# Performance work log

Hardware: AMD Instinct MI355X
Metric: run time of the kernel (lower is better)

The kernel has to match this reference:

```python
import jax, jax.numpy as jnp
import numpy as np

D_MODEL = 512
N_HEADS = 8
HEAD_DIM = D_MODEL // N_HEADS          # 64
ROTARY_DIM = HEAD_DIM // 2             # 32 (rotary_frac = 0.5)
MAX_SEQ_LEN = 512
EPS = 1e-6


def _rope_tables(seq_len, dtype=jnp.float32):
    inv_freq = 1.0 / (10000.0 ** (jnp.arange(0, ROTARY_DIM, 2, dtype=jnp.float32) / ROTARY_DIM))
    t = jnp.arange(seq_len, dtype=jnp.float32)
    freqs = jnp.outer(t, inv_freq)          # (T, ROTARY_DIM//2)
    return jnp.sin(freqs).astype(dtype), jnp.cos(freqs).astype(dtype)


def _apply_rope(x, sin, cos):
    # x: (R, H, T, Dh); rotate interleaved pairs of the first ROTARY_DIM dims
    rd = ROTARY_DIM
    x1 = x[..., :rd].reshape(*x.shape[:-1], rd // 2, 2)
    x2 = x[..., rd:]
    s = sin[None, None, :, :]
    c = cos[None, None, :, :]
    a, b = x1[..., 0], x1[..., 1]
    rot = jnp.stack([a * c - b * s, a * s + b * c], axis=-1).reshape(*x.shape[:-1], rd)
    return jnp.concatenate([rot, x2], axis=-1)


def setup_inputs() -> dict:
    key = jax.random.key(0)
    ks = jax.random.split(key, 8)
    B, T, N, D = 1, 384, 128, D_MODEL
    x = jax.random.normal(ks[0], (B, T, N, D), dtype=jnp.float32)
    neuron_pad_mask = jax.random.randint(ks[1], (B, N), 0, 2, dtype=jnp.int32)
    scale = 1.0 / np.sqrt(D)
    norm_w = jnp.ones((D,), dtype=jnp.float32)
    wq = jax.random.normal(ks[2], (D, D), dtype=jnp.float32) * scale
    wk = jax.random.normal(ks[3], (D, D), dtype=jnp.float32) * scale
    wv = jax.random.normal(ks[4], (D, D), dtype=jnp.float32) * scale
    wo = jax.random.normal(ks[5], (D, D), dtype=jnp.float32) * scale
    return {"x": x, "neuron_pad_mask": neuron_pad_mask, "norm_w": norm_w,
            "wq": wq, "wk": wk, "wv": wv, "wo": wo}


def reference(x, neuron_pad_mask, norm_w, wq, wk, wv, wo):
    B, T, N, D = x.shape
    H, Dh = N_HEADS, HEAD_DIM

    # RMSNorm over d_model
    xn = x * jax.lax.rsqrt(jnp.mean(x * x, axis=-1, keepdims=True) + EPS) * norm_w

    # (B,T,N,D) -> (B*N, T, D): each neuron is an independent causal timeline
    xt = jnp.transpose(xn, (0, 2, 1, 3)).reshape(B * N, T, D)
    res = xt

    # QKV projections (Linear, no bias: x @ W^T), split into heads -> (R,H,T,Dh)
    def to_bhld(y):
        return jnp.transpose(y.reshape(B * N, T, H, Dh), (0, 2, 1, 3))

    q = to_bhld(xt @ wq.T)
    k = to_bhld(xt @ wk.T)
    v = to_bhld(xt @ wv.T)

    sin, cos = _rope_tables(T, dtype=x.dtype)
    q = _apply_rope(q, sin, cos)
    k = _apply_rope(k, sin, cos)

    # Causal SDPA per row (scale = 1/sqrt(Dh), matching F.scaled_dot_product_attention)
    scores = jnp.einsum('rhtd,rhsd->rhts', q, k) / np.sqrt(Dh).astype(x.dtype)
    causal = jnp.tril(jnp.ones((T, T), dtype=bool))
    scores = jnp.where(causal[None, None], scores, jnp.finfo(scores.dtype).min)
    attn = jax.nn.softmax(scores, axis=-1)
    out = jnp.einsum('rhts,rhsd->rhtd', attn, v)            # (R,H,T,Dh)
    out = jnp.transpose(out, (0, 2, 1, 3)).reshape(B * N, T, D)

    # Only valid (non-padded) neuron rows receive attention output (others stay 0)
    valid = (neuron_pad_mask.reshape(-1) != 0)
    out = jnp.where(valid[:, None, None], out, jnp.zeros((), dtype=out.dtype))

    out = out + res
    out = jnp.transpose(out.reshape(B, N, T, D), (0, 2, 1, 3))  # (B,T,N,D)
    return out @ wo.T
```

## Files before the change

kernel.cpp:

```cpp
#include <hip/hip_runtime.h>
#include <hip/hip_bf16.h>
#include <stdint.h>

typedef __bf16 bf16x8 __attribute__((ext_vector_type(8)));
typedef float f32x4 __attribute__((ext_vector_type(4)));

static constexpr int T_SEQ  = 384;
static constexpr int NNEUR  = 128;
static constexpr int DMODEL = 512;
static constexpr int NROWS  = NNEUR * T_SEQ;
static constexpr float ROPE_C = 0.8304820237218406f;

__device__ __forceinline__ float bf2f(unsigned short u) {
  union { unsigned int i; float f; } x; x.i = ((unsigned int)u) << 16; return x.f;
}
__device__ __forceinline__ unsigned short f2bf(float f) {
  union { float f; unsigned int i; } x; x.f = f;
  unsigned int i = x.i;
  i += 0x7FFFu + ((i >> 16) & 1u);
  return (unsigned short)(i >> 16);
}
__device__ __forceinline__ float fast_exp2(float x) {
#if __has_builtin(__builtin_amdgcn_exp2f)
  return __builtin_amdgcn_exp2f(x);
#else
  return exp2f(x);
#endif
}

__device__ __forceinline__ void async_copy16(const unsigned short* g, unsigned short* l) {
  auto gp = reinterpret_cast<const __attribute__((address_space(1))) unsigned int*>(
      reinterpret_cast<uintptr_t>(g));
  auto lp = reinterpret_cast<__attribute__((address_space(3))) unsigned int*>(
      reinterpret_cast<uintptr_t>(l));
  __builtin_amdgcn_global_load_lds(gp, lp, 16, 0, 0);
}

__global__ __launch_bounds__(256) void cvt_w_kernel(
    const float* __restrict__ w0, const float* __restrict__ w1,
    const float* __restrict__ w2, const float* __restrict__ w3,
    unsigned short* __restrict__ o0, unsigned short* __restrict__ o1,
    unsigned short* __restrict__ o2, unsigned short* __restrict__ o3)
{
  const float* w; unsigned short* o;
  switch (blockIdx.y) {
    case 0:  w = w0; o = o0; break;
    case 1:  w = w1; o = o1; break;
    case 2:  w = w2; o = o2; break;
    default: w = w3; o = o3; break;
  }
  int i = (blockIdx.x * 256 + threadIdx.x) * 4;
  float4 v = *reinterpret_cast<const float4*>(w + i);
  union { unsigned short u[4]; uint2 v2; } p;
  p.u[0] = f2bf(v.x); p.u[1] = f2bf(v.y); p.u[2] = f2bf(v.z); p.u[3] = f2bf(v.w);
  *reinterpret_cast<uint2*>(o + i) = p.v2;
}

__global__ __launch_bounds__(256) void rope_tab_kernel(float2* __restrict__ tab) {
  int idx = blockIdx.x * 256 + threadIdx.x;
  int t = idx >> 4, i = idx & 15;
  float ang = (float)t * exp2f(-(float)i * ROPE_C);
  float s, c; sincosf(ang, &s, &c);
  tab[idx] = make_float2(s, c);
}

__global__ __launch_bounds__(256) void rmsnorm_kernel(
    const float* __restrict__ x, const float* __restrict__ nw,
    unsigned short* __restrict__ xt)
{
  int wave = threadIdx.x >> 6, lane = threadIdx.x & 63;
  int rid = blockIdx.x * 4 + wave;
  int t = rid >> 7, n = rid & 127;
  const float* row = x + (size_t)rid * DMODEL;
  float4 v0 = *reinterpret_cast<const float4*>(row + lane * 8);
  float4 v1 = *reinterpret_cast<const float4*>(row + lane * 8 + 4);
  float ss = v0.x*v0.x + v0.y*v0.y + v0.z*v0.z + v0.w*v0.w
           + v1.x*v1.x + v1.y*v1.y + v1.z*v1.z + v1.w*v1.w;
  #pragma unroll
  for (int off = 32; off; off >>= 1) ss += __shfl_xor(ss, off);
  float sc = rsqrtf(ss * (1.0f / DMODEL) + 1e-6f);
  float4 w0 = *reinterpret_cast<const float4*>(nw + lane * 8);
  float4 w1 = *reinterpret_cast<const float4*>(nw + lane * 8 + 4);
  union { unsigned short u[8]; uint4 v; } p;
  p.u[0] = f2bf(v0.x * sc * w0.x); p.u[1] = f2bf(v0.y * sc * w0.y);
  p.u[2] = f2bf(v0.z * sc * w0.z); p.u[3] = f2bf(v0.w * sc * w0.w);
  p.u[4] = f2bf(v1.x * sc * w1.x); p.u[5] = f2bf(v1.y * sc * w1.y);
  p.u[6] = f2bf(v1.z * sc * w1.z); p.u[7] = f2bf(v1.w * sc * w1.w);
  *reinterpret_cast<uint4*>(xt + ((size_t)n * T_SEQ + t) * DMODEL + lane * 8) = p.v;
}

template <int MODE, typename OutT>
__global__ __launch_bounds__(512, 4) void gemm_k(
    const unsigned short* __restrict__ A,
    const unsigned short* __restrict__ B,
    OutT* __restrict__ C,
    const float2* __restrict__ tab,
    const int* __restrict__ pad)
{
  __shared__ alignas(16) unsigned short Sh[2][12288];
  const int tid  = threadIdx.x;
  const int wave = tid >> 6, lane = tid & 63;
  const int l15  = lane & 15, quad = lane >> 4;
  const int wm = (wave >> 1) * 64, wn = (wave & 1) * 64;

  constexpr int GX = (MODE == 2) ? 8 : (MODE == 3) ? 2 : 4;
  constexpr int GY = (MODE == 3) ? 384 : 192;
  constexpr int NB = GX * GY;
  constexpr int CH = NB / 8;
  const int lin = (int)blockIdx.y * GX + (int)blockIdx.x;
  const int swz = (lin & 7) * CH + (lin >> 3);
  const int bx  = swz % GX, by = swz / GX;

  size_t m0; int n0;
  if constexpr (MODE == 3) { m0 = (size_t)bx * 256; n0 = by * 128; }
  else                     { m0 = (size_t)by * 256; n0 = bx * 128; }

  if constexpr (MODE == 2) {
    int nfirst = (int)(m0 / 384);
    int nlast  = (int)((m0 + 255) / 384);
    if (pad[nfirst] == 0 && pad[nlast] == 0) return;
  }
  if constexpr (MODE == 3) {
    if (pad[n0 / 384] == 0) return;
  }

  const int r4 = tid >> 2;
  const int c4 = tid & 3;
  const int gc = c4 ^ (r4 & 3);
  const unsigned short* ga = A + (m0 + r4) * 512 + gc * 8;
  const unsigned short* gb = B + ((size_t)n0 + r4) * 512 + gc * 8;

  const int pc = (quad ^ (l15 & 3)) * 8;

  auto STAGE = [&](int kk, int b) {
    const unsigned short* gak = ga + kk * 32;
    unsigned short* base = &Sh[b][0];
    async_copy16(gak,             base + tid * 8);
    async_copy16(gak + 128 * 512, base + 4096 + tid * 8);
    async_copy16(gb + kk * 32,    base + 8192 + tid * 8);
  };

  f32x4 acc[4][4] = {};
  auto COMPUTE = [&](int b) {
    const unsigned short* base = &Sh[b][0];
    bf16x8 a[4], bb[4];
    #pragma unroll
    for (int i = 0; i < 4; ++i)
      a[i] = *reinterpret_cast<const bf16x8*>(&base[(wm + i * 16 + l15) * 32 + pc]);
    #pragma unroll
    for (int j = 0; j < 4; ++j)
      bb[j] = *reinterpret_cast<const bf16x8*>(&base[8192 + (wn + j * 16 + l15) * 32 + pc]);
    #pragma unroll
    for (int i = 0; i < 4; ++i)
      #pragma unroll
      for (int j = 0; j < 4; ++j)
        acc[i][j] = __builtin_amdgcn_mfma_f32_16x16x32_bf16(a[i], bb[j], acc[i][j], 0, 0, 0);
  };

  STAGE(0, 0);
  #pragma unroll 2
  for (int kk = 0; kk < 15; ++kk) {
    const int b = kk & 1;
    STAGE(kk + 1, b ^ 1);
    asm volatile("s_waitcnt vmcnt(3)" ::: "memory");
    __builtin_amdgcn_s_barrier();
    __builtin_amdgcn_sched_barrier(0);
    COMPUTE(b);
    __builtin_amdgcn_sched_barrier(0);
    __builtin_amdgcn_s_barrier();
    __builtin_amdgcn_sched_barrier(0);
  }
  asm volatile("s_waitcnt vmcnt(0)" ::: "memory");
  __builtin_amdgcn_s_barrier();
  __builtin_amdgcn_sched_barrier(0);
  COMPUTE(1);

  if constexpr (MODE == 3) {
    #pragma unroll
    for (int j = 0; j < 4; ++j) {
      int xbase = n0 + wn + j * 16;
      int nn    = xbase / 384;
      int bloc  = xbase - nn * 384;
      int off64 = (bloc >> 6) * 64 + ((bloc >> 4) & 3);
      #pragma unroll
      for (int i = 0; i < 4; ++i)
        #pragma unroll
        for (int r = 0; r < 4; ++r) {
          int dout = (int)m0 + wm + i * 16 + quad * 4 + r;
          C[((size_t)nn * 512 + dout) * 384 + off64 + l15 * 4] = f2bf(acc[i][j][r]);
        }
    }
  } else {
    OutT* Cb = C;
    int ncol0 = n0 + wn;
    if constexpr (MODE == 2) {
      int sec = n0 >> 9;
      Cb = C + (size_t)sec * NROWS * 512;
      ncol0 = (n0 & 511) + wn;
    }
    #pragma unroll
    for (int i = 0; i < 4; ++i) {
      #pragma unroll
      for (int r = 0; r < 4; ++r) {
        size_t grow = m0 + wm + i * 16 + quad * 4 + r;
        int t = (int)(grow % 384);
        #pragma unroll
        for (int j = 0; j < 4; ++j) {
          float v = acc[i][j][r];
          int col = ncol0 + j * 16 + l15;
          if constexpr (MODE == 2) {
            if (((ncol0 + j * 16) & 63) < 32) {
              float part = __shfl_xor(v, 1);
              float2 scv = tab[t * 16 + ((col & 63) >> 1)];
              v = (l15 & 1) ? (part * scv.x + v * scv.y)
                            : (v * scv.y - part * scv.x);
            }
            Cb[grow * 512 + col] = f2bf(v);
          } else {
            Cb[grow * 512 + col] = v;
          }
        }
      }
    }
  }
}

__global__ __launch_bounds__(256, 4) void attn_kernel(
    const unsigned short* __restrict__ qb,
    const unsigned short* __restrict__ kb,
    const unsigned short* __restrict__ vt,
    const unsigned short* __restrict__ xt,
    const int* __restrict__ pad,
    unsigned short* __restrict__ y)
{
  const int lin = (int)blockIdx.x + 6 * ((int)blockIdx.y + 8 * (int)blockIdx.z);
  const int swz = (lin & 7) * 768 + (lin >> 3);
  const int qt  = swz % 6;
  const int rem = swz / 6;
  const int h   = rem & 7;
  const int n   = rem >> 3;

  const int tid  = threadIdx.x;

  if (pad[n] == 0) {
    int tq = qt * 64 + (tid >> 2);
    int d  = h * 64 + (tid & 3) * 16;
    const uint4* src = reinterpret_cast<const uint4*>(
        &xt[((size_t)n * T_SEQ + tq) * 512 + d]);
    uint4* dst = reinterpret_cast<uint4*>(
        &y[((size_t)tq * NNEUR + n) * 512 + d]);
    dst[0] = src[0];
    dst[1] = src[1];
    return;
  }

  __shared__ alignas(16) unsigned short Qs[64 * 64];
  __shared__ alignas(16) unsigned short Ks[64 * 64];
  __shared__ alignas(16) unsigned short VTs[64 * 64];
  __shared__ alignas(16) unsigned short Ps[4][16][72];

  const int wave = tid >> 6, lane = tid & 63;
  const int l15  = lane & 15, quad = lane >> 4;
  const int lrow = lane >> 3, lchunk = (lane & 7) ^ ((lane >> 3) & 7);
  const float C2 = 0.18033688011112042f;

  const unsigned short* gq =
      qb + ((size_t)n * T_SEQ + qt * 64 + wave * 16 + lrow) * 512 + h * 64 + lchunk * 8;
  async_copy16(gq,           &Qs[(wave * 16) * 64]);
  async_copy16(gq + 8 * 512, &Qs[(wave * 16 + 8) * 64]);

  const unsigned short* gk0 =
      kb + ((size_t)n * T_SEQ + wave * 16 + lrow) * 512 + h * 64 + lchunk * 8;
  const unsigned short* gv0 =
      vt + ((size_t)n * 512 + h * 64 + wave * 16 + lrow) * 384 + lchunk * 8;

  float lsum[4] = {0.f, 0.f, 0.f, 0.f};
  f32x4 oacc[4] = {};

  for (int kt = 0; kt <= qt; ++kt) {
    async_copy16(gk0 + (size_t)(kt * 64) * 512,     &Ks[(wave * 16) * 64]);
    async_copy16(gk0 + (size_t)(kt * 64 + 8) * 512, &Ks[(wave * 16 + 8) * 64]);
    async_copy16(gv0 + kt * 64,                     &VTs[(wave * 16) * 64]);
    async_copy16(gv0 + kt * 64 + 8 * 384,           &VTs[(wave * 16 + 8) * 64]);
    __syncthreads();

    f32x4 sc4[4] = {};
    #pragma unroll
    for (int kc = 0; kc < 2; ++kc) {
      const int pc = ((kc * 4 + quad) ^ (l15 & 7)) * 8;
      bf16x8 aq = *reinterpret_cast<const bf16x8*>(&Qs[(wave * 16 + l15) * 64 + pc]);
      #pragma unroll
      for (int tc = 0; tc < 4; ++tc) {
        bf16x8 bk = *reinterpret_cast<const bf16x8*>(&Ks[(tc * 16 + l15) * 64 + pc]);
        sc4[tc] = __builtin_amdgcn_mfma_f32_16x16x32_bf16(aq, bk, sc4[tc], 0, 0, 0);
      }
    }
    const bool diag = (kt == qt);
    float ps[4][4];
    #pragma unroll
    for (int tc = 0; tc < 4; ++tc)
      #pragma unroll
      for (int r = 0; r < 4; ++r) {
        float p = fast_exp2(sc4[tc][r] * C2 - 16.0f);
        if (diag && (tc * 16 + l15 > wave * 16 + quad * 4 + r)) p = 0.f;
        lsum[r] += p;
        ps[tc][r] = p;
      }
    #pragma unroll
    for (int r = 0; r < 4; ++r) {
      union { float f; unsigned int u; } a0, a1, a2, a3;
      a0.f = ps[0][r]; a1.f = ps[1][r]; a2.f = ps[2][r]; a3.f = ps[3][r];
      uint2 pk;
      pk.x = (a1.u & 0xffff0000u) | (a0.u >> 16);
      pk.y = (a3.u & 0xffff0000u) | (a2.u >> 16);
      *reinterpret_cast<uint2*>(&Ps[wave][quad * 4 + r][l15 * 4]) = pk;
    }
    #pragma unroll
    for (int kc = 0; kc < 2; ++kc) {
      const int pc = ((kc * 4 + quad) ^ (l15 & 7)) * 8;
      bf16x8 ap = *reinterpret_cast<const bf16x8*>(&Ps[wave][l15][kc * 32 + quad * 8]);
      #pragma unroll
      for (int dt = 0; dt < 4; ++dt) {
        bf16x8 bv = *reinterpret_cast<const bf16x8*>(&VTs[(dt * 16 + l15) * 64 + pc]);
        oacc[dt] = __builtin_amdgcn_mfma_f32_16x16x32_bf16(ap, bv, oacc[dt], 0, 0, 0);
      }
    }
    __syncthreads();
  }

  float inv[4];
  #pragma unroll
  for (int r = 0; r < 4; ++r) {
    float l = lsum[r];
    l += __shfl_xor(l, 1);
    l += __shfl_xor(l, 2);
    l += __shfl_xor(l, 4);
    l += __shfl_xor(l, 8);
    inv[r] = 1.0f / l;
  }
  #pragma unroll
  for (int dt = 0; dt < 4; ++dt)
    #pragma unroll
    for (int r = 0; r < 4; ++r) {
      int tq = qt * 64 + wave * 16 + quad * 4 + r;
      int d  = h * 64 + dt * 16 + l15;
      float val = oacc[dt][r] * inv[r];
      float res = bf2f(xt[((size_t)n * T_SEQ + tq) * 512 + d]);
      y[((size_t)tq * NNEUR + n) * 512 + d] = f2bf(val + res);
    }
}

extern "C" void kernel_launch(void* const* d_in, const int* in_sizes, int n_in,
                              void* d_out, int out_size, void* d_ws, size_t ws_size,
                              hipStream_t stream) {
  const float* x   = (const float*)d_in[0];
  const int*   pad = (const int*)d_in[1];
  const float* nw  = (const float*)d_in[2];
  const float* wq  = (const float*)d_in[3];
  const float* wk  = (const float*)d_in[4];
  const float* wv  = (const float*)d_in[5];
  const float* wo  = (const float*)d_in[6];
  float* out = (float*)d_out;

  char* ws = (char*)d_ws;
  size_t off = 0;
  auto alloc = [&](size_t bytes) { void* p = ws + off; off += (bytes + 255) & ~(size_t)255; return p; };
  const size_t WELEM  = (size_t)512 * 512;
  const size_t MBYTES = (size_t)NROWS * 512 * 2;
  unsigned short* wqkv_bf = (unsigned short*)alloc(WELEM * 3 * 2);
  unsigned short* wo_bf   = (unsigned short*)alloc(WELEM * 2);
  float2*         rtab    = (float2*)alloc(384 * 16 * sizeof(float2));
  unsigned short* xt_bf   = (unsigned short*)alloc(MBYTES);
  unsigned short* qk_buf  = (unsigned short*)alloc(MBYTES * 2);
  unsigned short* vt_buf  = (unsigned short*)alloc(MBYTES);
  unsigned short* y_buf   = (unsigned short*)alloc(MBYTES);

  cvt_w_kernel<<<dim3(256, 4), 256, 0, stream>>>(
      wq, wk, wv, wo,
      wqkv_bf, wqkv_bf + WELEM, wqkv_bf + 2 * WELEM, wo_bf);
  rope_tab_kernel<<<24, 256, 0, stream>>>(rtab);
  rmsnorm_kernel<<<NROWS / 4, 256, 0, stream>>>(x, nw, xt_bf);
  gemm_k<2, unsigned short><<<dim3(8, NROWS / 256), 512, 0, stream>>>(
      xt_bf, wqkv_bf, qk_buf, rtab, pad);
  gemm_k<3, unsigned short><<<dim3(2, NROWS / 128), 512, 0, stream>>>(
      wqkv_bf + 2 * WELEM, xt_bf, vt_buf, nullptr, pad);
  attn_kernel<<<dim3(6, 8, 128), 256, 0, stream>>>(
      qk_buf, qk_buf + (size_t)NROWS * 512, vt_buf, xt_bf, pad, y_buf);
  gemm_k<0, float><<<dim3(4, NROWS / 256), 512, 0, stream>>>(
      y_buf, wo_bf, out, nullptr, pad);
}
```

Measured before the change: 352.8 us.

## Enlarge attention query tile to 128 rows to reuse K/V tiles

After: 347.9 us. Within noise of the previous version (-1.4%).

```diff
diff --git a/kernel.cpp b/kernel.cpp
--- a/kernel.cpp
+++ b/kernel.cpp
@@ -233,28 +233,32 @@
     const int* __restrict__ pad,
     unsigned short* __restrict__ y)
 {
-  const int lin = (int)blockIdx.x + 6 * ((int)blockIdx.y + 8 * (int)blockIdx.z);
-  const int swz = (lin & 7) * 768 + (lin >> 3);
-  const int qt  = swz % 6;
-  const int rem = swz / 6;
+  const int lin = (int)blockIdx.x + 3 * ((int)blockIdx.y + 8 * (int)blockIdx.z);
+  const int swz = (lin & 7) * 384 + (lin >> 3);
+  const int qtb = swz % 3;
+  const int rem = swz / 3;
   const int h   = rem & 7;
   const int n   = rem >> 3;
 
   const int tid  = threadIdx.x;
 
   if (pad[n] == 0) {
-    int tq = qt * 64 + (tid >> 2);
+    int rb = tid >> 2;
     int d  = h * 64 + (tid & 3) * 16;
-    const uint4* src = reinterpret_cast<const uint4*>(
-        &xt[((size_t)n * T_SEQ + tq) * 512 + d]);
-    uint4* dst = reinterpret_cast<uint4*>(
-        &y[((size_t)tq * NNEUR + n) * 512 + d]);
-    dst[0] = src[0];
-    dst[1] = src[1];
+    #pragma unroll
+    for (int rr = 0; rr < 128; rr += 64) {
+      int tq = qtb * 128 + rr + rb;
+      const uint4* src = reinterpret_cast<const uint4*>(
+          &xt[((size_t)n * T_SEQ + tq) * 512 + d]);
+      uint4* dst = reinterpret_cast<uint4*>(
+          &y[((size_t)tq * NNEUR + n) * 512 + d]);
+      dst[0] = src[0];
+      dst[1] = src[1];
+    }
     return;
   }
 
-  __shared__ alignas(16) unsigned short Qs[64 * 64];
+  __shared__ alignas(16) unsigned short Qs[128 * 64];
   __shared__ alignas(16) unsigned short Ks[64 * 64];
   __shared__ alignas(16) unsigned short VTs[64 * 64];
   __shared__ alignas(16) unsigned short Ps[4][16][72];
@@ -265,89 +269,120 @@
   const float C2 = 0.18033688011112042f;
 
   const unsigned short* gq =
-      qb + ((size_t)n * T_SEQ + qt * 64 + wave * 16 + lrow) * 512 + h * 64 + lchunk * 8;
-  async_copy16(gq,           &Qs[(wave * 16) * 64]);
-  async_copy16(gq + 8 * 512, &Qs[(wave * 16 + 8) * 64]);
+      qb + ((size_t)n * T_SEQ + qtb * 128 + wave * 32 + lrow) * 512 + h * 64 + lchunk * 8;
+  #pragma unroll
+  for (int rr = 0; rr < 4; ++rr)
+    async_copy16(gq + (size_t)(rr * 8) * 512, &Qs[(wave * 32 + rr * 8) * 64]);
 
   const unsigned short* gk0 =
       kb + ((size_t)n * T_SEQ + wave * 16 + lrow) * 512 + h * 64 + lchunk * 8;
   const unsigned short* gv0 =
       vt + ((size_t)n * 512 + h * 64 + wave * 16 + lrow) * 384 + lchunk * 8;
 
-  float lsum[4] = {0.f, 0.f, 0.f, 0.f};
-  f32x4 oacc[4] = {};
-
-  for (int kt = 0; kt <= qt; ++kt) {
-    async_copy16(gk0 + (size_t)(kt * 64) * 512,     &Ks[(wave * 16) * 64]);
-    async_copy16(gk0 + (size_t)(kt * 64 + 8) * 512, &Ks[(wave * 16 + 8) * 64]);
-    async_copy16(gv0 + kt * 64,                     &VTs[(wave * 16) * 64]);
-    async_copy16(gv0 + kt * 64 + 8 * 384,           &VTs[(wave * 16 + 8) * 64]);
-    __syncthreads();
-
-    f32x4 sc4[4] = {};
+  const int nkt = 2 * qtb + 2;
+
+  float lsum[2][4] = {};
+  f32x4 oacc[2][4] = {};
+
+  async_copy16(gk0,           &Ks[(wave * 16) * 64]);
+  async_copy16(gk0 + 8 * 512, &Ks[(wave * 16 + 8) * 64]);
+  async_copy16(gv0,           &VTs[(wave * 16) * 64]);
+  async_copy16(gv0 + 8 * 384, &VTs[(wave * 16 + 8) * 64]);
+  __syncthreads();
+
+  bf16x8 aq[2][2];
+  #pragma unroll
+  for (int s = 0; s < 2; ++s)
     #pragma unroll
     for (int kc = 0; kc < 2; ++kc) {
-      const int pc = ((kc * 4 + quad) ^ (l15 & 7)) * 8;
-      bf16x8 aq = *reinterpret_cast<const bf16x8*>(&Qs[(wave * 16 + l15) * 64 + pc]);
-      #pragma unroll
-      for (int tc = 0; tc < 4; ++tc) {
-        bf16x8 bk = *reinterpret_cast<const bf16x8*>(&Ks[(tc * 16 + l15) * 64 + pc]);
-        sc4[tc] = __builtin_amdgcn_mfma_f32_16x16x32_bf16(aq, bk, sc4[tc], 0, 0, 0);
+      const int pcq = ((kc * 4 + quad) ^ (l15 & 7)) * 8;
+      aq[s][kc] = *reinterpret_cast<const bf16x8*>(
+          &Qs[(wave * 32 + s * 16 + l15) * 64 + pcq]);
+    }
+
+  for (int kt = 0; kt < nkt; ++kt) {
+    #pragma unroll
+    for (int s = 0; s < 2; ++s) {
+      const int qsub = qtb * 128 + wave * 32 + s * 16;
+      if (kt * 64 > qsub + 15) continue;
+
+      f32x4 sc4[4] = {};
+      #pragma unroll
+      for (int kc = 0; kc < 2; ++kc) {
+        const int pc = ((kc * 4 + quad) ^ (l15 & 7)) * 8;
+        #pragma unroll
+        for (int tc = 0; tc < 4; ++tc) {
+          bf16x8 bk = *reinterpret_cast<const bf16x8*>(&Ks[(tc * 16 + l15) * 64 + pc]);
+          sc4[tc] = __builtin_amdgcn_mfma_f32_16x16x32_bf16(aq[s][kc], bk, sc4[tc], 0, 0, 0);
+        }
       }
-    }
-    const bool diag = (kt == qt);
-    float ps[4][4];
-    #pragma unroll
-    for (int tc = 0; tc < 4; ++tc)
+      float ps_[4][4];
+      #pragma unroll
+      for (int tc = 0; tc < 4; ++tc)
+        #pragma unroll
+        for (int r = 0; r < 4; ++r) {
+          float p = fast_exp2(sc4[tc][r] * C2 - 16.0f);
+          int kglob = kt * 64 + tc * 16 + l15;
+          int qglob = qsub + quad * 4 + r;
+          if (kglob > qglob) p = 0.f;
+          lsum[s][r] += p;
+          ps_[tc][r] = p;
+        }
       #pragma unroll
       for (int r = 0; r < 4; ++r) {
-        float p = fast_exp2(sc4[tc][r] * C2 - 16.0f);
-        if (diag && (tc * 16 + l15 > wave * 16 + quad * 4 + r)) p = 0.f;
-        lsum[r] += p;
-        ps[tc][r] = p;
+        union { float f; unsigned int u; } a0, a1, a2, a3;
+        a0.f = ps_[0][r]; a1.f = ps_[1][r]; a2.f = ps_[2][r]; a3.f = ps_[3][r];
+        uint2 pk;
+        pk.x = (a1.u & 0xffff0000u) | (a0.u >> 16);
+        pk.y = (a3.u & 0xffff0000u) | (a2.u >> 16);
+        *reinterpret_cast<uint2*>(&Ps[wave][quad * 4 + r][l15 * 4]) = pk;
       }
+      #pragma unroll
+      for (int kc = 0; kc < 2; ++kc) {
+        const int pc = ((kc * 4 + quad) ^ (l15 & 7)) * 8;
+        bf16x8 ap = *reinterpret_cast<const bf16x8*>(&Ps[wave][l15][kc * 32 + quad * 8]);
+        #pragma unroll
+        for (int dt = 0; dt < 4; ++dt) {
+          bf16x8 bv = *reinterpret_cast<const bf16x8*>(&VTs[(dt * 16 + l15) * 64 + pc]);
+          oacc[s][dt] = __builtin_amdgcn_mfma_f32_16x16x32_bf16(ap, bv, oacc[s][dt], 0, 0, 0);
+        }
+      }
+    }
+    if (kt + 1 < nkt) {
+      __syncthreads();
+      const size_t ko = (size_t)(kt + 1) * 64;
+      async_copy16(gk0 + ko * 512,                 &Ks[(wave * 16) * 64]);
+      async_copy16(gk0 + (ko + 8) * 512,           &Ks[(wave * 16 + 8) * 64]);
+      async_copy16(gv0 + (kt + 1) * 64,            &VTs[(wave * 16) * 64]);
+      async_copy16(gv0 + (kt + 1) * 64 + 8 * 384,  &VTs[(wave * 16 + 8) * 64]);
+      __syncthreads();
+    }
+  }
+
+  float inv[2][4];
+  #pragma unroll
+  for (int s = 0; s < 2; ++s)
     #pragma unroll
     for (int r = 0; r < 4; ++r) {
-      union { float f; unsigned int u; } a0, a1, a2, a3;
-      a0.f = ps[0][r]; a1.f = ps[1][r]; a2.f = ps[2][r]; a3.f = ps[3][r];
-      uint2 pk;
-      pk.x = (a1.u & 0xffff0000u) | (a0.u >> 16);
-      pk.y = (a3.u & 0xffff0000u) | (a2.u >> 16);
-      *reinterpret_cast<uint2*>(&Ps[wave][quad * 4 + r][l15 * 4]) = pk;
-    }
-    #pragma unroll
-    for (int kc = 0; kc < 2; ++kc) {
-      const int pc = ((kc * 4 + quad) ^ (l15 & 7)) * 8;
-      bf16x8 ap = *reinterpret_cast<const bf16x8*>(&Ps[wave][l15][kc * 32 + quad * 8]);
-      #pragma unroll
-      for (int dt = 0; dt < 4; ++dt) {
-        bf16x8 bv = *reinterpret_cast<const bf16x8*>(&VTs[(dt * 16 + l15) * 64 + pc]);
-        oacc[dt] = __builtin_amdgcn_mfma_f32_16x16x32_bf16(ap, bv, oacc[dt], 0, 0, 0);
+      float l = lsum[s][r];
+      l += __shfl_xor(l, 1);
+      l += __shfl_xor(l, 2);
+      l += __shfl_xor(l, 4);
+      l += __shfl_xor(l, 8);
+      inv[s][r] = 1.0f / l;
+    }
+  #pragma unroll
+  for (int s = 0; s < 2; ++s)
+    #pragma unroll
+    for (int dt = 0; dt < 4; ++dt)
+      #pragma unroll
+      for (int r = 0; r < 4; ++r) {
+        int tq = qtb * 128 + wave * 32 + s * 16 + quad * 4 + r;
+        int d  = h * 64 + dt * 16 + l15;
+        float val = oacc[s][dt][r] * inv[s][r];
+        float res = bf2f(xt[((size_t)n * T_SEQ + tq) * 512 + d]);
+        y[((size_t)tq * NNEUR + n) * 512 + d] = f2bf(val + res);
       }
-    }
-    __syncthreads();
-  }
-
-  float inv[4];
-  #pragma unroll
-  for (int r = 0; r < 4; ++r) {
-    float l = lsum[r];
-    l += __shfl_xor(l, 1);
-    l += __shfl_xor(l, 2);
-    l += __shfl_xor(l, 4);
-    l += __shfl_xor(l, 8);
-    inv[r] = 1.0f / l;
-  }
-  #pragma unroll
-  for (int dt = 0; dt < 4; ++dt)
-    #pragma unroll
-    for (int r = 0; r < 4; ++r) {
-      int tq = qt * 64 + wave * 16 + quad * 4 + r;
-      int d  = h * 64 + dt * 16 + l15;
-      float val = oacc[dt][r] * inv[r];
-      float res = bf2f(xt[((size_t)n * T_SEQ + tq) * 512 + d]);
-      y[((size_t)tq * NNEUR + n) * 512 + d] = f2bf(val + res);
-    }
 }
 
 extern "C" void kernel_launch(void* const* d_in, const int* in_sizes, int n_in,
@@ -384,7 +419,7 @@
       xt_bf, wqkv_bf, qk_buf, rtab, pad);
   gemm_k<3, unsigned short><<<dim3(2, NROWS / 128), 512, 0, stream>>>(
       wqkv_bf + 2 * WELEM, xt_bf, vt_buf, nullptr, pad);
-  attn_kernel<<<dim3(6, 8, 128), 256, 0, stream>>>(
+  attn_kernel<<<dim3(3, 8, 128), 256, 0, stream>>>(
       qk_buf, qk_buf + (size_t)NROWS * 512, vt_buf, xt_bf, pad, y_buf);
   gemm_k<0, float><<<dim3(4, NROWS / 256), 512, 0, stream>>>(
       y_buf, wo_bf, out, nullptr, pad);
```
